# Performance work log

Measured on AMD Instinct MI355X. Metric: run time of the kernel, lower is better.

## Reference

```python
import jax, jax.numpy as jnp
import numpy as np

EMBED = 768
HEADS = 12
HEAD_DIM = EMBED // HEADS
B, S = 1, 4096


def setup_inputs() -> dict:
    key = jax.random.key(0)
    ks = jax.random.split(key, 8)
    values = jax.random.normal(ks[0], (B, S, EMBED), dtype=jnp.float32)
    keys_in = jax.random.normal(ks[1], (B, S, EMBED), dtype=jnp.float32)
    queries = jax.random.normal(ks[2], (B, S, EMBED), dtype=jnp.float32)
    # causal mask: 1.0 where attention is disallowed (gets * -1e9)
    mask = jnp.triu(jnp.ones((S, S), dtype=jnp.float32), k=1)[None, None, :, :]
    sc = 1.0 / np.sqrt(EMBED)
    W_q = jax.random.normal(ks[3], (EMBED, EMBED), dtype=jnp.float32) * sc
    W_k = jax.random.normal(ks[4], (EMBED, EMBED), dtype=jnp.float32) * sc
    W_v = jax.random.normal(ks[5], (EMBED, EMBED), dtype=jnp.float32) * sc
    W_o = jax.random.normal(ks[6], (EMBED, EMBED), dtype=jnp.float32) * sc
    b_o = jnp.zeros((EMBED,), dtype=jnp.float32)
    return {"values": values, "keys": keys_in, "queries": queries, "mask": mask,
            "W_q": W_q, "W_k": W_k, "W_v": W_v, "W_o": W_o, "b_o": b_o}


def reference(values, keys, queries, mask, W_q, W_k, W_v, W_o, b_o):
    N, S_, _ = queries.shape
    # linear projections (Dense, no bias)
    q = queries @ W_q  # [N, S, E]
    k = keys @ W_k
    v = values @ W_v
    # split heads -> [N, H, S, Dh]
    def split(x):
        return x.reshape(N, S_, HEADS, HEAD_DIM).transpose(0, 2, 1, 3)
    q, k, v = split(q), split(k), split(v)
    scores = jnp.einsum('nhqd,nhkd->nhqk', q, k) / jnp.sqrt(
        jnp.asarray(HEAD_DIM, dtype=q.dtype))
    scores = scores + mask * (-1e9)
    attn = jax.nn.softmax(scores, axis=-1)
    out = jnp.einsum('nhqk,nhkd->nhqd', attn, v)  # [N, H, S, Dh]
    out = out.transpose(0, 2, 1, 3).reshape(N, S_, EMBED)
    return out @ W_o + b_o
```

## Files before the change

### kernel.cpp

```cpp
#include <hip/hip_runtime.h>

#define S_LEN 4096
#define EMB   768
#define NH    12
#define DH    64

typedef __attribute__((ext_vector_type(8))) short bf16x8;
typedef __attribute__((ext_vector_type(4))) float f32x4;

__device__ __forceinline__ unsigned short f2bf(float f) {
    union { float f; unsigned u; } v; v.f = f;
    unsigned r = v.u + 0x7fffu + ((v.u >> 16) & 1u);
    return (unsigned short)(r >> 16);
}
__device__ __forceinline__ float bf2f(unsigned short u) {
    union { unsigned u; float f; } v; v.u = (unsigned)u << 16; return v.f;
}
__device__ __forceinline__ f32x4 mfma16(bf16x8 a, bf16x8 b, f32x4 c) {
    return __builtin_amdgcn_mfma_f32_16x16x32_bf16(a, b, c, 0, 0, 0);
}
__device__ __forceinline__ void async16(unsigned short* lds, const unsigned short* g) {
    __builtin_amdgcn_global_load_lds(
        (const __attribute__((address_space(1))) unsigned int*)(const void*)g,
        (__attribute__((address_space(3))) unsigned int*)(void*)lds, 16, 0, 0);
}

__global__ void prep_w(const float* __restrict__ Wq, const float* __restrict__ Wk,
                       const float* __restrict__ Wv, const float* __restrict__ Wo,
                       unsigned short* __restrict__ WT) {
    __shared__ float tile[64][65];
    int z = blockIdx.z;
    const float* W = (z == 0) ? Wq : (z == 1) ? Wk : (z == 2) ? Wv : Wo;
    unsigned short* out = WT + (size_t)z * EMB * EMB;
    int k0 = blockIdx.x * 64, n0 = blockIdx.y * 64;
    int t = threadIdx.x;
    int row = t >> 2, c = (t & 3) * 16;
    const float4* src = (const float4*)(W + (size_t)(k0 + row) * EMB + n0 + c);
#pragma unroll
    for (int i = 0; i < 4; i++) {
        float4 v = src[i];
        tile[row][c + i * 4 + 0] = v.x; tile[row][c + i * 4 + 1] = v.y;
        tile[row][c + i * 4 + 2] = v.z; tile[row][c + i * 4 + 3] = v.w;
    }
    __syncthreads();
    unsigned short tmp[16] __attribute__((aligned(16)));
#pragma unroll
    for (int i = 0; i < 16; i++) tmp[i] = f2bf(tile[c + i][row]);
    int4* dst = (int4*)(out + (size_t)(n0 + row) * EMB + k0 + c);
    dst[0] = *(int4*)&tmp[0];
    dst[1] = *(int4*)&tmp[8];
}

__global__ __launch_bounds__(256) void gemm_qkv(const float* __restrict__ Aq,
                                                const float* __restrict__ Ak,
                                                const float* __restrict__ Av,
                                                const unsigned short* __restrict__ WT,
                                                unsigned short* __restrict__ Qh,
                                                unsigned short* __restrict__ Kh,
                                                unsigned short* __restrict__ Vt) {
    __shared__ unsigned short As[128 * 32];
    __shared__ unsigned short Bs[128 * 32];
    int m0 = blockIdx.x * 128;
    int ng = blockIdx.y * 128;
    int z  = ng / EMB;
    int n0 = ng - z * EMB;
    const float* A = (z == 0) ? Aq : (z == 1) ? Ak : Av;
    const unsigned short* Bt = WT + (size_t)z * EMB * EMB;

    int t = threadIdx.x, lane = t & 63, wv = t >> 6, quad = lane >> 4, l16 = lane & 15;
    int wm = wv >> 1, wn = wv & 1;
    int srow = t >> 2, scol = (t & 3) * 8;

    f32x4 acc[4][4] = {};
    const float*          ga0 = A  + (size_t)(m0 + srow) * EMB + scol;
    const float*          ga1 = ga0 + (size_t)64 * EMB;
    const unsigned short* gb0 = Bt + (size_t)(n0 + srow) * EMB + scol;
    const unsigned short* gb1 = gb0 + (size_t)64 * EMB;

    for (int k0 = 0; k0 < EMB; k0 += 32) {
        async16(&Bs[t * 8], gb0 + k0);
        async16(&Bs[2048 + t * 8], gb1 + k0);
        float4 a00 = *(const float4*)(ga0 + k0);
        float4 a01 = *(const float4*)(ga0 + k0 + 4);
        float4 a10 = *(const float4*)(ga1 + k0);
        float4 a11 = *(const float4*)(ga1 + k0 + 4);
        unsigned short ta[8] __attribute__((aligned(16)));
        ta[0] = f2bf(a00.x); ta[1] = f2bf(a00.y); ta[2] = f2bf(a00.z); ta[3] = f2bf(a00.w);
        ta[4] = f2bf(a01.x); ta[5] = f2bf(a01.y); ta[6] = f2bf(a01.z); ta[7] = f2bf(a01.w);
        *(int4*)&As[srow * 32 + scol] = *(int4*)ta;
        ta[0] = f2bf(a10.x); ta[1] = f2bf(a10.y); ta[2] = f2bf(a10.z); ta[3] = f2bf(a10.w);
        ta[4] = f2bf(a11.x); ta[5] = f2bf(a11.y); ta[6] = f2bf(a11.z); ta[7] = f2bf(a11.w);
        *(int4*)&As[(srow + 64) * 32 + scol] = *(int4*)ta;
        __syncthreads();
        bf16x8 fa[4], fb[4];
#pragma unroll
        for (int mi = 0; mi < 4; mi++)
            fa[mi] = *(bf16x8*)&As[(wm * 64 + mi * 16 + l16) * 32 + quad * 8];
#pragma unroll
        for (int ni = 0; ni < 4; ni++)
            fb[ni] = *(bf16x8*)&Bs[(wn * 64 + ni * 16 + l16) * 32 + quad * 8];
#pragma unroll
        for (int mi = 0; mi < 4; mi++)
#pragma unroll
            for (int ni = 0; ni < 4; ni++)
                acc[mi][ni] = mfma16(fa[mi], fb[ni], acc[mi][ni]);
        __syncthreads();
    }

    float sc = (z == 0) ? 0.125f : 1.0f;
#pragma unroll
    for (int mi = 0; mi < 4; mi++)
#pragma unroll
        for (int ni = 0; ni < 4; ni++)
#pragma unroll
            for (int r = 0; r < 4; r++) {
                int m = m0 + wm * 64 + mi * 16 + quad * 4 + r;
                int n = n0 + wn * 64 + ni * 16 + l16;
                int h = n >> 6, d = n & 63;
                unsigned short b = f2bf(acc[mi][ni][r] * sc);
                if (z == 2) Vt[((size_t)(h * DH + d)) * S_LEN + m] = b;
                else {
                    unsigned short* dst = z ? Kh : Qh;
                    dst[((size_t)(h * S_LEN + m)) * DH + d] = b;
                }
            }
}

__global__ __launch_bounds__(256) void attn_kernel(const unsigned short* __restrict__ Qh,
                                                   const unsigned short* __restrict__ Kh,
                                                   const unsigned short* __restrict__ Vt,
                                                   unsigned short* __restrict__ Opart,
                                                   float* __restrict__ Lpart) {
    __shared__ unsigned short Kls[64 * 72];
    __shared__ unsigned short Vls[64 * 72];
    __shared__ unsigned short Pls[4 * 16 * 72];

    int qb = blockIdx.x, h = blockIdx.y, chunk = blockIdx.z;
    int part = (h * 64 + qb) * 2 + chunk;
    unsigned short* opart = Opart + (size_t)part * 4096;
    float*          lpart = Lpart + (size_t)part * 64;

    int t = threadIdx.x, w = t >> 6, lane = t & 63, quad = lane >> 4, l16 = lane & 15;
    int ntiles = qb + 1, half = (ntiles + 1) >> 1;
    int jb = chunk ? half : 0, je = chunk ? ntiles : half;

    if (jb >= je) {
        int4 z4 = {0, 0, 0, 0};
        ((int4*)opart)[t] = z4;
        ((int4*)opart)[t + 256] = z4;
        if (t < 64) lpart[t] = 0.f;
        return;
    }

    int q0 = qb * 64;
    int lrow = t >> 2, lc = (t & 3) * 16;

    const unsigned short* qbase = Qh + ((size_t)(h * S_LEN + q0 + w * 16 + l16)) * DH + quad * 8;
    bf16x8 aQ0 = *(const bf16x8*)(qbase);
    bf16x8 aQ1 = *(const bf16x8*)(qbase + 32);

    f32x4 o[4] = {};
    float lsum[4] = {0.f, 0.f, 0.f, 0.f};

    const unsigned short* kbase = Kh + (size_t)h * S_LEN * DH;
    const unsigned short* vbase = Vt + ((size_t)h * DH + lrow) * S_LEN;

    for (int jt = jb; jt < je; jt++) {
        int j0 = jt * 64;
        __syncthreads();
        *(int4*)&Kls[lrow * 72 + lc]     = *(const int4*)(kbase + (size_t)(j0 + lrow) * DH + lc);
        *(int4*)&Kls[lrow * 72 + lc + 8] = *(const int4*)(kbase + (size_t)(j0 + lrow) * DH + lc + 8);
        *(int4*)&Vls[lrow * 72 + lc]     = *(const int4*)(vbase + j0 + lc);
        *(int4*)&Vls[lrow * 72 + lc + 8] = *(const int4*)(vbase + j0 + lc + 8);
        __syncthreads();

        f32x4 s[4];
#pragma unroll
        for (int nt = 0; nt < 4; nt++) {
            bf16x8 b0 = *(bf16x8*)&Kls[(nt * 16 + l16) * 72 + quad * 8];
            bf16x8 b1 = *(bf16x8*)&Kls[(nt * 16 + l16) * 72 + 32 + quad * 8];
            f32x4 zz = {};
            zz = mfma16(aQ0, b0, zz);
            zz = mfma16(aQ1, b1, zz);
            s[nt] = zz;
        }

        if (jt == qb) {
#pragma unroll
            for (int nt = 0; nt < 4; nt++) {
                int col = nt * 16 + l16;
#pragma unroll
                for (int r = 0; r < 4; r++) {
                    int row = w * 16 + quad * 4 + r;
                    if (col > row) s[nt][r] = -1e9f;
                }
            }
        }

        unsigned short pbits[4][4];
#pragma unroll
        for (int r = 0; r < 4; r++) {
            float p0 = __expf(s[0][r]);
            float p1 = __expf(s[1][r]);
            float p2 = __expf(s[2][r]);
            float p3 = __expf(s[3][r]);
            lsum[r] += (p0 + p1) + (p2 + p3);
            pbits[r][0] = f2bf(p0); pbits[r][1] = f2bf(p1);
            pbits[r][2] = f2bf(p2); pbits[r][3] = f2bf(p3);
        }

        unsigned short* pw = &Pls[(w * 16) * 72];
#pragma unroll
        for (int r = 0; r < 4; r++)
#pragma unroll
            for (int nt = 0; nt < 4; nt++)
                pw[(quad * 4 + r) * 72 + nt * 16 + l16] = pbits[r][nt];
        __asm__ volatile("s_waitcnt lgkmcnt(0)" ::: "memory");

        bf16x8 aP0 = *(bf16x8*)&Pls[(w * 16 + l16) * 72 + quad * 8];
        bf16x8 aP1 = *(bf16x8*)&Pls[(w * 16 + l16) * 72 + 32 + quad * 8];
#pragma unroll
        for (int nt = 0; nt < 4; nt++) {
            bf16x8 bv0 = *(bf16x8*)&Vls[(nt * 16 + l16) * 72 + quad * 8];
            bf16x8 bv1 = *(bf16x8*)&Vls[(nt * 16 + l16) * 72 + 32 + quad * 8];
            o[nt] = mfma16(aP0, bv0, o[nt]);
            o[nt] = mfma16(aP1, bv1, o[nt]);
        }
    }

#pragma unroll
    for (int r = 0; r < 4; r++) {
#pragma unroll
        for (int off = 8; off >= 1; off >>= 1) lsum[r] += __shfl_xor(lsum[r], off);
        int row = w * 16 + quad * 4 + r;
#pragma unroll
        for (int nt = 0; nt < 4; nt++)
            opart[row * 64 + nt * 16 + l16] = f2bf(o[nt][r]);
        if (l16 == 0) lpart[row] = lsum[r];
    }
}

__global__ __launch_bounds__(256) void gemm_out(const unsigned short* __restrict__ Opart,
                                                const float* __restrict__ Lpart,
                                                const unsigned short* __restrict__ WT,
                                                const float* __restrict__ bias,
                                                float* __restrict__ out) {
    __shared__ unsigned short As[128 * 32];
    __shared__ unsigned short Bs[128 * 32];
    int m0 = blockIdx.x * 128, n0 = blockIdx.y * 128;
    const unsigned short* Bt = WT + (size_t)3 * EMB * EMB;

    int t = threadIdx.x, lane = t & 63, wv = t >> 6, quad = lane >> 4, l16 = lane & 15;
    int wm = wv >> 1, wn = wv & 1;
    int srow = t >> 2, scol = (t & 3) * 8;
    int s0 = m0 + srow, s1 = s0 + 64;
    int qb0 = s0 >> 6, r0 = s0 & 63, qb1 = s1 >> 6, r1 = s1 & 63;

    f32x4 acc[4][4] = {};
    const unsigned short* gb0 = Bt + (size_t)(n0 + srow) * EMB + scol;
    const unsigned short* gb1 = gb0 + (size_t)64 * EMB;

    for (int k0 = 0; k0 < EMB; k0 += 32) {
        async16(&Bs[t * 8], gb0 + k0);
        async16(&Bs[2048 + t * 8], gb1 + k0);
        int e = k0 + scol, hh = e >> 6, d = e & 63;
        {
            size_t pbase = ((size_t)((hh * 64 + qb0) * 2)) * 4096 + (size_t)r0 * 64 + d;
            int4 x0 = *(const int4*)(Opart + pbase);
            int4 x1 = *(const int4*)(Opart + pbase + 4096);
            int lb = ((hh * 64 + qb0) * 2) * 64 + r0;
            float invl = 1.0f / (Lpart[lb] + Lpart[lb + 64]);
            unsigned short* pa = (unsigned short*)&x0;
            unsigned short* pb = (unsigned short*)&x1;
            unsigned short ta[8] __attribute__((aligned(16)));
#pragma unroll
            for (int i = 0; i < 8; i++)
                ta[i] = f2bf((bf2f(pa[i]) + bf2f(pb[i])) * invl);
            *(int4*)&As[srow * 32 + scol] = *(int4*)ta;
        }
        {
            size_t pbase = ((size_t)((hh * 64 + qb1) * 2)) * 4096 + (size_t)r1 * 64 + d;
            int4 x0 = *(const int4*)(Opart + pbase);
            int4 x1 = *(const int4*)(Opart + pbase + 4096);
            int lb = ((hh * 64 + qb1) * 2) * 64 + r1;
            float invl = 1.0f / (Lpart[lb] + Lpart[lb + 64]);
            unsigned short* pa = (unsigned short*)&x0;
            unsigned short* pb = (unsigned short*)&x1;
            unsigned short ta[8] __attribute__((aligned(16)));
#pragma unroll
            for (int i = 0; i < 8; i++)
                ta[i] = f2bf((bf2f(pa[i]) + bf2f(pb[i])) * invl);
            *(int4*)&As[(srow + 64) * 32 + scol] = *(int4*)ta;
        }
        __syncthreads();
        bf16x8 fa[4], fb[4];
#pragma unroll
        for (int mi = 0; mi < 4; mi++)
            fa[mi] = *(bf16x8*)&As[(wm * 64 + mi * 16 + l16) * 32 + quad * 8];
#pragma unroll
        for (int ni = 0; ni < 4; ni++)
            fb[ni] = *(bf16x8*)&Bs[(wn * 64 + ni * 16 + l16) * 32 + quad * 8];
#pragma unroll
        for (int mi = 0; mi < 4; mi++)
#pragma unroll
            for (int ni = 0; ni < 4; ni++)
                acc[mi][ni] = mfma16(fa[mi], fb[ni], acc[mi][ni]);
        __syncthreads();
    }

#pragma unroll
    for (int mi = 0; mi < 4; mi++)
#pragma unroll
        for (int ni = 0; ni < 4; ni++)
#pragma unroll
            for (int r = 0; r < 4; r++) {
                int m = m0 + wm * 64 + mi * 16 + quad * 4 + r;
                int n = n0 + wn * 64 + ni * 16 + l16;
                out[(size_t)m * EMB + n] = acc[mi][ni][r] + bias[n];
            }
}

extern "C" void kernel_launch(void* const* d_in, const int* in_sizes, int n_in,
                              void* d_out, int out_size, void* d_ws, size_t ws_size,
                              hipStream_t stream) {
    const float* values  = (const float*)d_in[0];
    const float* keys    = (const float*)d_in[1];
    const float* queries = (const float*)d_in[2];
    const float* Wq = (const float*)d_in[4];
    const float* Wk = (const float*)d_in[5];
    const float* Wv = (const float*)d_in[6];
    const float* Wo = (const float*)d_in[7];
    const float* bo = (const float*)d_in[8];

    char* ws = (char*)d_ws;
    unsigned short* WT = (unsigned short*)ws;
    unsigned short* Qh = (unsigned short*)(ws + 4718592);
    unsigned short* Kh = (unsigned short*)(ws + 11010048);
    unsigned short* Vt = (unsigned short*)(ws + 17301504);
    unsigned short* Op = (unsigned short*)(ws + 23592960);
    float*          Lp = (float*)(ws + 36175872);
    float* out = (float*)d_out;

    prep_w<<<dim3(12, 12, 4), 256, 0, stream>>>(Wq, Wk, Wv, Wo, WT);
    gemm_qkv<<<dim3(32, 18), 256, 0, stream>>>(queries, keys, values, WT, Qh, Kh, Vt);
    attn_kernel<<<dim3(64, 12, 2), 256, 0, stream>>>(Qh, Kh, Vt, Op, Lp);
    gemm_out<<<dim3(32, 6), 256, 0, stream>>>(Op, Lp, WT, bo, out);
}
```

Before: 299.8 us.

## Restructure pipeline: pre-convert inputs, double-buffered swizzled GEMMs, split-K attention with merge

Converts the fp32 activations to bf16 in a fused prep kernel alongside the weight transpose, so the QKV GEMM can stream bf16 tiles with async global-to-LDS loads into double-buffered, XOR-swizzled 64-wide K tiles. The attention kernel now covers 128-row query blocks split into chunks of up to 8 key tiles for load balance, double-buffers K/V in LDS, and uses packed bf16 conversion. A separate merge kernel combines the partials and normalizes, and the output GEMM then reads a plain bf16 O. This adds a launch plus extra conversion traffic in exchange for better latency hiding, fewer barriers and better balanced causal work.

```diff
diff --git a/kernel.cpp b/kernel.cpp
--- a/kernel.cpp
+++ b/kernel.cpp
@@ -5,6 +5,7 @@
 #define NH    12
 #define DH    64
 
+typedef unsigned short ushort_t;
 typedef __attribute__((ext_vector_type(8))) short bf16x8;
 typedef __attribute__((ext_vector_type(4))) float f32x4;
 
@@ -16,6 +17,11 @@
 __device__ __forceinline__ float bf2f(unsigned short u) {
     union { unsigned u; float f; } v; v.u = (unsigned)u << 16; return v.f;
 }
+__device__ __forceinline__ unsigned pk2(float lo, float hi) {
+    unsigned r;
+    asm("v_cvt_pk_bf16_f32 %0, %1, %2" : "=v"(r) : "v"(lo), "v"(hi));
+    return r;
+}
 __device__ __forceinline__ f32x4 mfma16(bf16x8 a, bf16x8 b, f32x4 c) {
     return __builtin_amdgcn_mfma_f32_16x16x32_bf16(a, b, c, 0, 0, 0);
 }
@@ -25,105 +31,142 @@
         (__attribute__((address_space(3))) unsigned int*)(void*)lds, 16, 0, 0);
 }
 
-__global__ void prep_w(const float* __restrict__ Wq, const float* __restrict__ Wk,
-                       const float* __restrict__ Wv, const float* __restrict__ Wo,
-                       unsigned short* __restrict__ WT) {
-    __shared__ float tile[64][65];
-    int z = blockIdx.z;
-    const float* W = (z == 0) ? Wq : (z == 1) ? Wk : (z == 2) ? Wv : Wo;
-    unsigned short* out = WT + (size_t)z * EMB * EMB;
-    int k0 = blockIdx.x * 64, n0 = blockIdx.y * 64;
-    int t = threadIdx.x;
-    int row = t >> 2, c = (t & 3) * 16;
-    const float4* src = (const float4*)(W + (size_t)(k0 + row) * EMB + n0 + c);
-#pragma unroll
-    for (int i = 0; i < 4; i++) {
-        float4 v = src[i];
-        tile[row][c + i * 4 + 0] = v.x; tile[row][c + i * 4 + 1] = v.y;
-        tile[row][c + i * 4 + 2] = v.z; tile[row][c + i * 4 + 3] = v.w;
-    }
-    __syncthreads();
-    unsigned short tmp[16] __attribute__((aligned(16)));
-#pragma unroll
-    for (int i = 0; i < 16; i++) tmp[i] = f2bf(tile[c + i][row]);
-    int4* dst = (int4*)(out + (size_t)(n0 + row) * EMB + k0 + c);
-    dst[0] = *(int4*)&tmp[0];
-    dst[1] = *(int4*)&tmp[8];
-}
-
-__global__ __launch_bounds__(256) void gemm_qkv(const float* __restrict__ Aq,
-                                                const float* __restrict__ Ak,
-                                                const float* __restrict__ Av,
+__global__ __launch_bounds__(256) void prep(const float* __restrict__ Wq, const float* __restrict__ Wk,
+                     const float* __restrict__ Wv, const float* __restrict__ Wo,
+                     const float* __restrict__ q_in, const float* __restrict__ k_in,
+                     const float* __restrict__ v_in,
+                     unsigned short* __restrict__ WT, unsigned short* __restrict__ conv) {
+    int bx = blockIdx.x, t = threadIdx.x;
+    if (bx < 576) {
+        __shared__ float tile[64][65];
+        int z = bx / 144, rem = bx % 144;
+        int k0 = (rem / 12) * 64, n0 = (rem % 12) * 64;
+        const float* W = (z == 0) ? Wq : (z == 1) ? Wk : (z == 2) ? Wv : Wo;
+        unsigned short* out = WT + (size_t)z * EMB * EMB;
+        int row = t >> 2, c = (t & 3) * 16;
+        const float4* src = (const float4*)(W + (size_t)(k0 + row) * EMB + n0 + c);
+#pragma unroll
+        for (int i = 0; i < 4; i++) {
+            float4 v = src[i];
+            tile[row][c + i * 4 + 0] = v.x; tile[row][c + i * 4 + 1] = v.y;
+            tile[row][c + i * 4 + 2] = v.z; tile[row][c + i * 4 + 3] = v.w;
+        }
+        __syncthreads();
+        unsigned short tmp[16] __attribute__((aligned(16)));
+#pragma unroll
+        for (int i = 0; i < 16; i++) tmp[i] = f2bf(tile[c + i][row]);
+        int4* dst = (int4*)(out + (size_t)(n0 + row) * EMB + k0 + c);
+        dst[0] = *(int4*)&tmp[0];
+        dst[1] = *(int4*)&tmp[8];
+    } else {
+        size_t idx = (size_t)(bx - 576) * 256 + t;
+        size_t e8 = idx * 8;
+        int z = (int)(e8 / 3145728);
+        size_t off = e8 - (size_t)z * 3145728;
+        const float* src = (z == 0) ? q_in : (z == 1) ? k_in : v_in;
+        float4 a = *(const float4*)(src + off);
+        float4 b = *(const float4*)(src + off + 4);
+        unsigned r[4];
+        r[0] = pk2(a.x, a.y); r[1] = pk2(a.z, a.w);
+        r[2] = pk2(b.x, b.y); r[3] = pk2(b.z, b.w);
+        *(int4*)(conv + e8) = *(int4*)r;
+    }
+}
+
+__global__ __launch_bounds__(256) void gemm_qkv(const unsigned short* __restrict__ conv,
                                                 const unsigned short* __restrict__ WT,
                                                 unsigned short* __restrict__ Qh,
                                                 unsigned short* __restrict__ Kh,
                                                 unsigned short* __restrict__ Vt) {
-    __shared__ unsigned short As[128 * 32];
-    __shared__ unsigned short Bs[128 * 32];
+    __shared__ unsigned short As[2][8192];
+    __shared__ unsigned short Bs[2][8192];
     int m0 = blockIdx.x * 128;
-    int ng = blockIdx.y * 128;
-    int z  = ng / EMB;
-    int n0 = ng - z * EMB;
-    const float* A = (z == 0) ? Aq : (z == 1) ? Ak : Av;
-    const unsigned short* Bt = WT + (size_t)z * EMB * EMB;
-
+    int z = blockIdx.y / 6, n0 = (blockIdx.y % 6) * 128;
+    const unsigned short* A  = conv + (size_t)z * 3145728;
+    const unsigned short* Bt = WT   + (size_t)z * 589824;
     int t = threadIdx.x, lane = t & 63, wv = t >> 6, quad = lane >> 4, l16 = lane & 15;
     int wm = wv >> 1, wn = wv & 1;
-    int srow = t >> 2, scol = (t & 3) * 8;
-
+    int c0 = (quad ^ (l16 & 7)) * 8, c1 = (((quad + 4) ^ (l16 & 7))) * 8;
+
+    const unsigned short* pa[4];
+    const unsigned short* pb[4];
+    int ldso[4];
+#pragma unroll
+    for (int a2 = 0; a2 < 4; a2++) {
+        int s1 = a2 * 256 + t, r = s1 >> 3, gc = (s1 & 7) ^ (r & 7);
+        pa[a2] = A  + (size_t)(m0 + r) * EMB + gc * 8;
+        pb[a2] = Bt + (size_t)(n0 + r) * EMB + gc * 8;
+        ldso[a2] = s1 * 8;
+    }
     f32x4 acc[4][4] = {};
-    const float*          ga0 = A  + (size_t)(m0 + srow) * EMB + scol;
-    const float*          ga1 = ga0 + (size_t)64 * EMB;
-    const unsigned short* gb0 = Bt + (size_t)(n0 + srow) * EMB + scol;
-    const unsigned short* gb1 = gb0 + (size_t)64 * EMB;
-
-    for (int k0 = 0; k0 < EMB; k0 += 32) {
-        async16(&Bs[t * 8], gb0 + k0);
-        async16(&Bs[2048 + t * 8], gb1 + k0);
-        float4 a00 = *(const float4*)(ga0 + k0);
-        float4 a01 = *(const float4*)(ga0 + k0 + 4);
-        float4 a10 = *(const float4*)(ga1 + k0);
-        float4 a11 = *(const float4*)(ga1 + k0 + 4);
-        unsigned short ta[8] __attribute__((aligned(16)));
-        ta[0] = f2bf(a00.x); ta[1] = f2bf(a00.y); ta[2] = f2bf(a00.z); ta[3] = f2bf(a00.w);
-        ta[4] = f2bf(a01.x); ta[5] = f2bf(a01.y); ta[6] = f2bf(a01.z); ta[7] = f2bf(a01.w);
-        *(int4*)&As[srow * 32 + scol] = *(int4*)ta;
-        ta[0] = f2bf(a10.x); ta[1] = f2bf(a10.y); ta[2] = f2bf(a10.z); ta[3] = f2bf(a10.w);
-        ta[4] = f2bf(a11.x); ta[5] = f2bf(a11.y); ta[6] = f2bf(a11.z); ta[7] = f2bf(a11.w);
-        *(int4*)&As[(srow + 64) * 32 + scol] = *(int4*)ta;
+
+#pragma unroll 1
+    for (int kt = 0; kt < 12; kt++) {
+        int buf = kt & 1;
+        if (kt == 0) {
+#pragma unroll
+            for (int a2 = 0; a2 < 4; a2++) {
+                async16(&As[0][ldso[a2]], pa[a2]); pa[a2] += 64;
+                async16(&Bs[0][ldso[a2]], pb[a2]); pb[a2] += 64;
+            }
+        }
         __syncthreads();
-        bf16x8 fa[4], fb[4];
+        if (kt < 11) {
+#pragma unroll
+            for (int a2 = 0; a2 < 4; a2++) {
+                async16(&As[buf ^ 1][ldso[a2]], pa[a2]); pa[a2] += 64;
+                async16(&Bs[buf ^ 1][ldso[a2]], pb[a2]); pb[a2] += 64;
+            }
+        }
+        bf16x8 fa[4][2], fb[4][2];
+#pragma unroll
+        for (int mi = 0; mi < 4; mi++) {
+            int row = wm * 64 + mi * 16 + l16;
+            fa[mi][0] = *(bf16x8*)&As[buf][row * 64 + c0];
+            fa[mi][1] = *(bf16x8*)&As[buf][row * 64 + c1];
+        }
+#pragma unroll
+        for (int ni = 0; ni < 4; ni++) {
+            int row = wn * 64 + ni * 16 + l16;
+            fb[ni][0] = *(bf16x8*)&Bs[buf][row * 64 + c0];
+            fb[ni][1] = *(bf16x8*)&Bs[buf][row * 64 + c1];
+        }
 #pragma unroll
         for (int mi = 0; mi < 4; mi++)
-            fa[mi] = *(bf16x8*)&As[(wm * 64 + mi * 16 + l16) * 32 + quad * 8];
-#pragma unroll
-        for (int ni = 0; ni < 4; ni++)
-            fb[ni] = *(bf16x8*)&Bs[(wn * 64 + ni * 16 + l16) * 32 + quad * 8];
+#pragma unroll
+            for (int ni = 0; ni < 4; ni++) {
+                acc[mi][ni] = mfma16(fa[mi][0], fb[ni][0], acc[mi][ni]);
+                acc[mi][ni] = mfma16(fa[mi][1], fb[ni][1], acc[mi][ni]);
+            }
+    }
+
+    if (z == 2) {
 #pragma unroll
         for (int mi = 0; mi < 4; mi++)
 #pragma unroll
-            for (int ni = 0; ni < 4; ni++)
-                acc[mi][ni] = mfma16(fa[mi], fb[ni], acc[mi][ni]);
-        __syncthreads();
-    }
-
-    float sc = (z == 0) ? 0.125f : 1.0f;
-#pragma unroll
-    for (int mi = 0; mi < 4; mi++)
-#pragma unroll
-        for (int ni = 0; ni < 4; ni++)
-#pragma unroll
-            for (int r = 0; r < 4; r++) {
-                int m = m0 + wm * 64 + mi * 16 + quad * 4 + r;
+            for (int ni = 0; ni < 4; ni++) {
+                int m = m0 + wm * 64 + mi * 16 + quad * 4;
                 int n = n0 + wn * 64 + ni * 16 + l16;
                 int h = n >> 6, d = n & 63;
-                unsigned short b = f2bf(acc[mi][ni][r] * sc);
-                if (z == 2) Vt[((size_t)(h * DH + d)) * S_LEN + m] = b;
-                else {
-                    unsigned short* dst = z ? Kh : Qh;
-                    dst[((size_t)(h * S_LEN + m)) * DH + d] = b;
+                uint2 val;
+                val.x = pk2(acc[mi][ni][0], acc[mi][ni][1]);
+                val.y = pk2(acc[mi][ni][2], acc[mi][ni][3]);
+                *(uint2*)&Vt[(size_t)(h * 64 + d) * S_LEN + m] = val;
+            }
+    } else {
+        unsigned short* dst = z ? Kh : Qh;
+        float sc = z ? 1.0f : 0.125f;
+#pragma unroll
+        for (int mi = 0; mi < 4; mi++)
+#pragma unroll
+            for (int ni = 0; ni < 4; ni++)
+#pragma unroll
+                for (int r = 0; r < 4; r++) {
+                    int m = m0 + wm * 64 + mi * 16 + quad * 4 + r;
+                    int n = n0 + wn * 64 + ni * 16 + l16;
+                    dst[((size_t)(n >> 6) * S_LEN + m) * 64 + (n & 63)] = f2bf(acc[mi][ni][r] * sc);
                 }
-            }
+    }
 }
 
 __global__ __launch_bounds__(256) void attn_kernel(const unsigned short* __restrict__ Qh,
@@ -131,183 +174,258 @@
                                                    const unsigned short* __restrict__ Vt,
                                                    unsigned short* __restrict__ Opart,
                                                    float* __restrict__ Lpart) {
-    __shared__ unsigned short Kls[64 * 72];
-    __shared__ unsigned short Vls[64 * 72];
-    __shared__ unsigned short Pls[4 * 16 * 72];
-
-    int qb = blockIdx.x, h = blockIdx.y, chunk = blockIdx.z;
-    int part = (h * 64 + qb) * 2 + chunk;
-    unsigned short* opart = Opart + (size_t)part * 4096;
-    float*          lpart = Lpart + (size_t)part * 64;
+    __shared__ unsigned short Kls[2][4096];
+    __shared__ unsigned short Vls[2][4096];
+    __shared__ unsigned short Pls[4 * 32 * 72];
+
+    int p = blockIdx.x, h = blockIdx.y;
+    int qb2 = 0, pre = 0;
+    while (pre + (qb2 >> 2) + 1 <= p) { pre += (qb2 >> 2) + 1; qb2++; }
+    int sp = p - pre;
+    int part = h * 144 + p;
+    int ntile = 2 * qb2 + 2;
+    int jb = sp * 8, je = min(jb + 8, ntile);
+    int q0 = qb2 << 7;
 
     int t = threadIdx.x, w = t >> 6, lane = t & 63, quad = lane >> 4, l16 = lane & 15;
-    int ntiles = qb + 1, half = (ntiles + 1) >> 1;
-    int jb = chunk ? half : 0, je = chunk ? ntiles : half;
-
-    if (jb >= je) {
-        int4 z4 = {0, 0, 0, 0};
-        ((int4*)opart)[t] = z4;
-        ((int4*)opart)[t + 256] = z4;
-        if (t < 64) lpart[t] = 0.f;
-        return;
-    }
-
-    int q0 = qb * 64;
-    int lrow = t >> 2, lc = (t & 3) * 16;
-
-    const unsigned short* qbase = Qh + ((size_t)(h * S_LEN + q0 + w * 16 + l16)) * DH + quad * 8;
-    bf16x8 aQ0 = *(const bf16x8*)(qbase);
-    bf16x8 aQ1 = *(const bf16x8*)(qbase + 32);
-
-    f32x4 o[4] = {};
-    float lsum[4] = {0.f, 0.f, 0.f, 0.f};
-
-    const unsigned short* kbase = Kh + (size_t)h * S_LEN * DH;
-    const unsigned short* vbase = Vt + ((size_t)h * DH + lrow) * S_LEN;
-
+    int rb = w * 32;
+    int c0 = (quad ^ (l16 & 7)) * 8, c1 = (((quad + 4) ^ (l16 & 7))) * 8;
+
+    const unsigned short* kb_ = Kh + (size_t)h * S_LEN * DH;
+    const unsigned short* vb_ = Vt + (size_t)h * S_LEN * DH;
+
+    bf16x8 aQ[2][2];
+#pragma unroll
+    for (int rg = 0; rg < 2; rg++)
+#pragma unroll
+        for (int kh = 0; kh < 2; kh++)
+            aQ[rg][kh] = *(const bf16x8*)(Qh + ((size_t)h * S_LEN + q0 + rb + rg * 16 + l16) * 64 + kh * 32 + quad * 8);
+
+    const unsigned short* pk_[2];
+    const unsigned short* pv_[2];
+    int ldso[2];
+#pragma unroll
+    for (int a2 = 0; a2 < 2; a2++) {
+        int s1 = a2 * 256 + t, r = s1 >> 3, gc = (s1 & 7) ^ (r & 7);
+        pk_[a2] = kb_ + (size_t)(jb * 64 + r) * 64 + gc * 8;
+        pv_[a2] = vb_ + (size_t)r * S_LEN + jb * 64 + gc * 8;
+        ldso[a2] = s1 * 8;
+    }
+
+    f32x4 o[4][2] = {};
+    float lsum[2][4] = {};
+    unsigned short* pwave = &Pls[w * 32 * 72];
+
+#pragma unroll 1
     for (int jt = jb; jt < je; jt++) {
-        int j0 = jt * 64;
+        int buf = (jt - jb) & 1;
+        if (jt == jb) {
+#pragma unroll
+            for (int a2 = 0; a2 < 2; a2++) {
+                async16(&Kls[0][ldso[a2]], pk_[a2]); pk_[a2] += 4096;
+                async16(&Vls[0][ldso[a2]], pv_[a2]); pv_[a2] += 64;
+            }
+        }
         __syncthreads();
-        *(int4*)&Kls[lrow * 72 + lc]     = *(const int4*)(kbase + (size_t)(j0 + lrow) * DH + lc);
-        *(int4*)&Kls[lrow * 72 + lc + 8] = *(const int4*)(kbase + (size_t)(j0 + lrow) * DH + lc + 8);
-        *(int4*)&Vls[lrow * 72 + lc]     = *(const int4*)(vbase + j0 + lc);
-        *(int4*)&Vls[lrow * 72 + lc + 8] = *(const int4*)(vbase + j0 + lc + 8);
-        __syncthreads();
-
-        f32x4 s[4];
-#pragma unroll
-        for (int nt = 0; nt < 4; nt++) {
-            bf16x8 b0 = *(bf16x8*)&Kls[(nt * 16 + l16) * 72 + quad * 8];
-            bf16x8 b1 = *(bf16x8*)&Kls[(nt * 16 + l16) * 72 + 32 + quad * 8];
-            f32x4 zz = {};
-            zz = mfma16(aQ0, b0, zz);
-            zz = mfma16(aQ1, b1, zz);
-            s[nt] = zz;
-        }
-
-        if (jt == qb) {
+        if (jt + 1 < je) {
+#pragma unroll
+            for (int a2 = 0; a2 < 2; a2++) {
+                async16(&Kls[buf ^ 1][ldso[a2]], pk_[a2]); pk_[a2] += 4096;
+                async16(&Vls[buf ^ 1][ldso[a2]], pv_[a2]); pv_[a2] += 64;
+            }
+        }
+        bool active = !(jt == 2 * qb2 + 1 && w < 2);
+        if (active) {
+            f32x4 s[2][4];
 #pragma unroll
             for (int nt = 0; nt < 4; nt++) {
-                int col = nt * 16 + l16;
-#pragma unroll
-                for (int r = 0; r < 4; r++) {
-                    int row = w * 16 + quad * 4 + r;
-                    if (col > row) s[nt][r] = -1e9f;
+                int row = nt * 16 + l16;
+                bf16x8 k0f = *(bf16x8*)&Kls[buf][row * 64 + c0];
+                bf16x8 k1f = *(bf16x8*)&Kls[buf][row * 64 + c1];
+#pragma unroll
+                for (int rg = 0; rg < 2; rg++) {
+                    f32x4 zz = {};
+                    zz = mfma16(aQ[rg][0], k0f, zz);
+                    zz = mfma16(aQ[rg][1], k1f, zz);
+                    s[rg][nt] = zz;
                 }
             }
-        }
-
-        unsigned short pbits[4][4];
+            if (jt >= 2 * qb2) {
+                int dlt = (jt - 2 * qb2) * 64;
+#pragma unroll
+                for (int rg = 0; rg < 2; rg++)
+#pragma unroll
+                    for (int nt = 0; nt < 4; nt++) {
+                        int col = nt * 16 + l16;
+#pragma unroll
+                        for (int r = 0; r < 4; r++) {
+                            int rel = rb + rg * 16 + quad * 4 + r - dlt;
+                            if (col > rel) s[rg][nt][r] = -1e9f;
+                        }
+                    }
+            }
+#pragma unroll
+            for (int rg = 0; rg < 2; rg++)
+#pragma unroll
+                for (int nt = 0; nt < 4; nt++) {
+                    float p0 = __expf(s[rg][nt][0]);
+                    float p1 = __expf(s[rg][nt][1]);
+                    float p2 = __expf(s[rg][nt][2]);
+                    float p3 = __expf(s[rg][nt][3]);
+                    lsum[rg][0] += p0; lsum[rg][1] += p1;
+                    lsum[rg][2] += p2; lsum[rg][3] += p3;
+                    unsigned pa2 = pk2(p0, p1), pb2 = pk2(p2, p3);
+                    unsigned short* pw = &pwave[(rg * 16 + quad * 4) * 72 + nt * 16 + l16];
+                    pw[0]       = (unsigned short)pa2;
+                    pw[72]      = (unsigned short)(pa2 >> 16);
+                    pw[144]     = (unsigned short)pb2;
+                    pw[216]     = (unsigned short)(pb2 >> 16);
+                }
+            asm volatile("s_waitcnt lgkmcnt(0)" ::: "memory");
+            bf16x8 bP[2][2];
+#pragma unroll
+            for (int ntq = 0; ntq < 2; ntq++) {
+                bP[ntq][0] = *(bf16x8*)&pwave[(ntq * 16 + l16) * 72 + quad * 8];
+                bP[ntq][1] = *(bf16x8*)&pwave[(ntq * 16 + l16) * 72 + 32 + quad * 8];
+            }
+#pragma unroll
+            for (int mt = 0; mt < 4; mt++) {
+                int row = mt * 16 + l16;
+                bf16x8 v0f = *(bf16x8*)&Vls[buf][row * 64 + c0];
+                bf16x8 v1f = *(bf16x8*)&Vls[buf][row * 64 + c1];
+#pragma unroll
+                for (int ntq = 0; ntq < 2; ntq++) {
+                    o[mt][ntq] = mfma16(v0f, bP[ntq][0], o[mt][ntq]);
+                    o[mt][ntq] = mfma16(v1f, bP[ntq][1], o[mt][ntq]);
+                }
+            }
+        }
+    }
+
+    unsigned short* op = Opart + (size_t)part * 8192;
+#pragma unroll
+    for (int mt = 0; mt < 4; mt++)
+#pragma unroll
+        for (int ntq = 0; ntq < 2; ntq++) {
+            uint2 val;
+            val.x = pk2(o[mt][ntq][0], o[mt][ntq][1]);
+            val.y = pk2(o[mt][ntq][2], o[mt][ntq][3]);
+            int q = rb + ntq * 16 + l16;
+            int d = mt * 16 + quad * 4;
+            *(uint2*)&op[q * 64 + d] = val;
+        }
+    float* lp = Lpart + (size_t)part * 128;
+#pragma unroll
+    for (int rg = 0; rg < 2; rg++)
 #pragma unroll
         for (int r = 0; r < 4; r++) {
-            float p0 = __expf(s[0][r]);
-            float p1 = __expf(s[1][r]);
-            float p2 = __expf(s[2][r]);
-            float p3 = __expf(s[3][r]);
-            lsum[r] += (p0 + p1) + (p2 + p3);
-            pbits[r][0] = f2bf(p0); pbits[r][1] = f2bf(p1);
-            pbits[r][2] = f2bf(p2); pbits[r][3] = f2bf(p3);
-        }
-
-        unsigned short* pw = &Pls[(w * 16) * 72];
-#pragma unroll
-        for (int r = 0; r < 4; r++)
-#pragma unroll
-            for (int nt = 0; nt < 4; nt++)
-                pw[(quad * 4 + r) * 72 + nt * 16 + l16] = pbits[r][nt];
-        __asm__ volatile("s_waitcnt lgkmcnt(0)" ::: "memory");
-
-        bf16x8 aP0 = *(bf16x8*)&Pls[(w * 16 + l16) * 72 + quad * 8];
-        bf16x8 aP1 = *(bf16x8*)&Pls[(w * 16 + l16) * 72 + 32 + quad * 8];
-#pragma unroll
-        for (int nt = 0; nt < 4; nt++) {
-            bf16x8 bv0 = *(bf16x8*)&Vls[(nt * 16 + l16) * 72 + quad * 8];
-            bf16x8 bv1 = *(bf16x8*)&Vls[(nt * 16 + l16) * 72 + 32 + quad * 8];
-            o[nt] = mfma16(aP0, bv0, o[nt]);
-            o[nt] = mfma16(aP1, bv1, o[nt]);
-        }
-    }
-
-#pragma unroll
-    for (int r = 0; r < 4; r++) {
-#pragma unroll
-        for (int off = 8; off >= 1; off >>= 1) lsum[r] += __shfl_xor(lsum[r], off);
-        int row = w * 16 + quad * 4 + r;
-#pragma unroll
-        for (int nt = 0; nt < 4; nt++)
-            opart[row * 64 + nt * 16 + l16] = f2bf(o[nt][r]);
-        if (l16 == 0) lpart[row] = lsum[r];
-    }
-}
-
-__global__ __launch_bounds__(256) void gemm_out(const unsigned short* __restrict__ Opart,
-                                                const float* __restrict__ Lpart,
+            float v = lsum[rg][r];
+            v += __shfl_xor(v, 8); v += __shfl_xor(v, 4);
+            v += __shfl_xor(v, 2); v += __shfl_xor(v, 1);
+            if (l16 == 0) lp[rb + rg * 16 + quad * 4 + r] = v;
+        }
+}
+
+__global__ __launch_bounds__(256) void merge(const unsigned short* __restrict__ Opart,
+                                             const float* __restrict__ Lpart,
+                                             unsigned short* __restrict__ O) {
+    int qb2 = blockIdx.x, h = blockIdx.y;
+    int a = qb2 >> 2, b = qb2 & 3;
+    int pre = qb2 + 2 * a * (a - 1) + a * b;
+    int cnt = a + 1;
+    int pbase = h * 144 + pre;
+    int t = threadIdx.x, row = t >> 1, ch = (t & 1) * 32;
+
+    float acc[32] = {};
+    float ls = 0.f;
+    const unsigned short* src = Opart + (size_t)pbase * 8192 + row * 64 + ch;
+    for (int p2 = 0; p2 < cnt; p2++) {
+        ls += Lpart[(size_t)(pbase + p2) * 128 + row];
+        const int4* s4 = (const int4*)(src + (size_t)p2 * 8192);
+#pragma unroll
+        for (int i = 0; i < 4; i++) {
+            int4 x = s4[i];
+            const unsigned short* xs = (const unsigned short*)&x;
+#pragma unroll
+            for (int j = 0; j < 8; j++) acc[i * 8 + j] += bf2f(xs[j]);
+        }
+    }
+    float inv = 1.0f / ls;
+    unsigned out[16];
+#pragma unroll
+    for (int i = 0; i < 16; i++) out[i] = pk2(acc[2 * i] * inv, acc[2 * i + 1] * inv);
+    int4* dst = (int4*)(O + (size_t)(qb2 * 128 + row) * EMB + h * 64 + ch);
+#pragma unroll
+    for (int i = 0; i < 4; i++) dst[i] = *(int4*)&out[i * 4];
+}
+
+__global__ __launch_bounds__(256) void gemm_out(const unsigned short* __restrict__ O,
                                                 const unsigned short* __restrict__ WT,
                                                 const float* __restrict__ bias,
                                                 float* __restrict__ out) {
-    __shared__ unsigned short As[128 * 32];
-    __shared__ unsigned short Bs[128 * 32];
+    __shared__ unsigned short As[2][8192];
+    __shared__ unsigned short Bs[2][8192];
     int m0 = blockIdx.x * 128, n0 = blockIdx.y * 128;
-    const unsigned short* Bt = WT + (size_t)3 * EMB * EMB;
-
+    const unsigned short* Bt = WT + (size_t)3 * 589824;
     int t = threadIdx.x, lane = t & 63, wv = t >> 6, quad = lane >> 4, l16 = lane & 15;
     int wm = wv >> 1, wn = wv & 1;
-    int srow = t >> 2, scol = (t & 3) * 8;
-    int s0 = m0 + srow, s1 = s0 + 64;
-    int qb0 = s0 >> 6, r0 = s0 & 63, qb1 = s1 >> 6, r1 = s1 & 63;
-
+    int c0 = (quad ^ (l16 & 7)) * 8, c1 = (((quad + 4) ^ (l16 & 7))) * 8;
+
+    const unsigned short* pa[4];
+    const unsigned short* pb[4];
+    int ldso[4];
+#pragma unroll
+    for (int a2 = 0; a2 < 4; a2++) {
+        int s1 = a2 * 256 + t, r = s1 >> 3, gc = (s1 & 7) ^ (r & 7);
+        pa[a2] = O  + (size_t)(m0 + r) * EMB + gc * 8;
+        pb[a2] = Bt + (size_t)(n0 + r) * EMB + gc * 8;
+        ldso[a2] = s1 * 8;
+    }
     f32x4 acc[4][4] = {};
-    const unsigned short* gb0 = Bt + (size_t)(n0 + srow) * EMB + scol;
-    const unsigned short* gb1 = gb0 + (size_t)64 * EMB;
-
-    for (int k0 = 0; k0 < EMB; k0 += 32) {
-        async16(&Bs[t * 8], gb0 + k0);
-        async16(&Bs[2048 + t * 8], gb1 + k0);
-        int e = k0 + scol, hh = e >> 6, d = e & 63;
-        {
-            size_t pbase = ((size_t)((hh * 64 + qb0) * 2)) * 4096 + (size_t)r0 * 64 + d;
-            int4 x0 = *(const int4*)(Opart + pbase);
-            int4 x1 = *(const int4*)(Opart + pbase + 4096);
-            int lb = ((hh * 64 + qb0) * 2) * 64 + r0;
-            float invl = 1.0f / (Lpart[lb] + Lpart[lb + 64]);
-            unsigned short* pa = (unsigned short*)&x0;
-            unsigned short* pb = (unsigned short*)&x1;
-            unsigned short ta[8] __attribute__((aligned(16)));
-#pragma unroll
-            for (int i = 0; i < 8; i++)
-                ta[i] = f2bf((bf2f(pa[i]) + bf2f(pb[i])) * invl);
-            *(int4*)&As[srow * 32 + scol] = *(int4*)ta;
-        }
-        {
-            size_t pbase = ((size_t)((hh * 64 + qb1) * 2)) * 4096 + (size_t)r1 * 64 + d;
-            int4 x0 = *(const int4*)(Opart + pbase);
-            int4 x1 = *(const int4*)(Opart + pbase + 4096);
-            int lb = ((hh * 64 + qb1) * 2) * 64 + r1;
-            float invl = 1.0f / (Lpart[lb] + Lpart[lb + 64]);
-            unsigned short* pa = (unsigned short*)&x0;
-            unsigned short* pb = (unsigned short*)&x1;
-            unsigned short ta[8] __attribute__((aligned(16)));
-#pragma unroll
-            for (int i = 0; i < 8; i++)
-                ta[i] = f2bf((bf2f(pa[i]) + bf2f(pb[i])) * invl);
-            *(int4*)&As[(srow + 64) * 32 + scol] = *(int4*)ta;
+
+#pragma unroll 1
+    for (int kt = 0; kt < 12; kt++) {
+        int buf = kt & 1;
+        if (kt == 0) {
+#pragma unroll
+            for (int a2 = 0; a2 < 4; a2++) {
+                async16(&As[0][ldso[a2]], pa[a2]); pa[a2] += 64;
+                async16(&Bs[0][ldso[a2]], pb[a2]); pb[a2] += 64;
+            }
         }
         __syncthreads();
-        bf16x8 fa[4], fb[4];
+        if (kt < 11) {
+#pragma unroll
+            for (int a2 = 0; a2 < 4; a2++) {
+                async16(&As[buf ^ 1][ldso[a2]], pa[a2]); pa[a2] += 64;
+                async16(&Bs[buf ^ 1][ldso[a2]], pb[a2]); pb[a2] += 64;
+            }
+        }
+        bf16x8 fa[4][2], fb[4][2];
+#pragma unroll
+        for (int mi = 0; mi < 4; mi++) {
+            int row = wm * 64 + mi * 16 + l16;
+            fa[mi][0] = *(bf16x8*)&As[buf][row * 64 + c0];
+            fa[mi][1] = *(bf16x8*)&As[buf][row * 64 + c1];
+        }
+#pragma unroll
+        for (int ni = 0; ni < 4; ni++) {
+            int row = wn * 64 + ni * 16 + l16;
+            fb[ni][0] = *(bf16x8*)&Bs[buf][row * 64 + c0];
+            fb[ni][1] = *(bf16x8*)&Bs[buf][row * 64 + c1];
+        }
 #pragma unroll
         for (int mi = 0; mi < 4; mi++)
-            fa[mi] = *(bf16x8*)&As[(wm * 64 + mi * 16 + l16) * 32 + quad * 8];
-#pragma unroll
-        for (int ni = 0; ni < 4; ni++)
-            fb[ni] = *(bf16x8*)&Bs[(wn * 64 + ni * 16 + l16) * 32 + quad * 8];
-#pragma unroll
-        for (int mi = 0; mi < 4; mi++)
-#pragma unroll
-            for (int ni = 0; ni < 4; ni++)
-                acc[mi][ni] = mfma16(fa[mi], fb[ni], acc[mi][ni]);
-        __syncthreads();
-    }
-
+#pragma unroll
+            for (int ni = 0; ni < 4; ni++) {
+                acc[mi][ni] = mfma16(fa[mi][0], fb[ni][0], acc[mi][ni]);
+                acc[mi][ni] = mfma16(fa[mi][1], fb[ni][1], acc[mi][ni]);
+            }
+    }
+
+    float bv[4];
+#pragma unroll
+    for (int ni = 0; ni < 4; ni++) bv[ni] = bias[n0 + wn * 64 + ni * 16 + l16];
 #pragma unroll
     for (int mi = 0; mi < 4; mi++)
 #pragma unroll
@@ -316,7 +434,7 @@
             for (int r = 0; r < 4; r++) {
                 int m = m0 + wm * 64 + mi * 16 + quad * 4 + r;
                 int n = n0 + wn * 64 + ni * 16 + l16;
-                out[(size_t)m * EMB + n] = acc[mi][ni][r] + bias[n];
+                out[(size_t)m * EMB + n] = acc[mi][ni][r] + bv[ni];
             }
 }
 
@@ -337,12 +455,15 @@
     unsigned short* Qh = (unsigned short*)(ws + 4718592);
     unsigned short* Kh = (unsigned short*)(ws + 11010048);
     unsigned short* Vt = (unsigned short*)(ws + 17301504);
-    unsigned short* Op = (unsigned short*)(ws + 23592960);
-    float*          Lp = (float*)(ws + 36175872);
+    unsigned short* O  = (unsigned short*)(ws + 23592960);
+    unsigned short* conv = (unsigned short*)(ws + 29884416);
+    unsigned short* Op   = (unsigned short*)(ws + 29884416);
+    float*          Lp   = (float*)(ws + 29884416 + 28311552);
     float* out = (float*)d_out;
 
-    prep_w<<<dim3(12, 12, 4), 256, 0, stream>>>(Wq, Wk, Wv, Wo, WT);
-    gemm_qkv<<<dim3(32, 18), 256, 0, stream>>>(queries, keys, values, WT, Qh, Kh, Vt);
-    attn_kernel<<<dim3(64, 12, 2), 256, 0, stream>>>(Qh, Kh, Vt, Op, Lp);
-    gemm_out<<<dim3(32, 6), 256, 0, stream>>>(Op, Lp, WT, bo, out);
-}
+    prep<<<dim3(5184), 256, 0, stream>>>(Wq, Wk, Wv, Wo, queries, keys, values, WT, conv);
+    gemm_qkv<<<dim3(32, 18), 256, 0, stream>>>(conv, WT, Qh, Kh, Vt);
+    attn_kernel<<<dim3(144, 12), 256, 0, stream>>>(Qh, Kh, Vt, Op, Lp);
+    merge<<<dim3(32, 12), 256, 0, stream>>>(Op, Lp, O);
+    gemm_out<<<dim3(32, 6), 256, 0, stream>>>(O, WT, bo, out);
+}
```

New measurement: 248.7 us. 1.21x faster.
